# Optimization experiments

Hardware: AMD Instinct MI355X
Metric: run time of the kernel (lower is better)

## Reference

```python
import jax, jax.numpy as jnp
import numpy as np

N_HEADS = 8
D_HEAD = 64


def setup_inputs() -> dict:
    key = jax.random.key(0)
    ks = jax.random.split(key, 7)
    B, Sq, Dm = 16, 4096, 512
    Skv, Dc = 77, 768
    inner = N_HEADS * D_HEAD  # 512
    s = lambda d: 1.0 / np.sqrt(d)
    return {
        "x": jax.random.normal(ks[0], (B, Sq, Dm), jnp.float32),
        "context": jax.random.normal(ks[1], (B, Skv, Dc), jnp.float32),
        "Wq": jax.random.normal(ks[2], (Dm, inner), jnp.float32) * s(Dm),
        "Wk": jax.random.normal(ks[3], (Dc, inner), jnp.float32) * s(Dc),
        "Wv": jax.random.normal(ks[4], (Dc, inner), jnp.float32) * s(Dc),
        "Wout": jax.random.normal(ks[5], (inner, inner), jnp.float32) * s(inner),
        "bout": jnp.zeros((inner,), jnp.float32),
    }


def reference(x, context, Wq, Wk, Wv, Wout, bout):
    B, Sq, _ = x.shape
    Skv = context.shape[1]
    scale = D_HEAD ** (-0.5)
    # projections (no bias)
    q = (x @ Wq).reshape(B, Sq, N_HEADS, D_HEAD)
    k = (context @ Wk).reshape(B, Skv, N_HEADS, D_HEAD)
    v = (context @ Wv).reshape(B, Skv, N_HEADS, D_HEAD)
    # scores: [B, H, Sq, Skv]
    score = jnp.einsum("bqhd,bkhd->bhqk", q, k) * scale
    weights = jax.nn.softmax(score, axis=-1)
    attn = jnp.einsum("bhqk,bkhd->bqhd", weights, v)
    h = attn.reshape(B, Sq, N_HEADS * D_HEAD)
    return h @ Wout + bout
```

## Files before the change

kernel.cpp:

```cpp
#include <hip/hip_runtime.h>


typedef unsigned short u16;
typedef unsigned int u32;
typedef _Float16 f16;
typedef __attribute__((ext_vector_type(8))) _Float16 half8;
typedef __attribute__((ext_vector_type(4))) _Float16 half4;
typedef __attribute__((ext_vector_type(4))) float f32x4;

__device__ __forceinline__ f32x4 mfma16h(half8 a, half8 b, f32x4 c) {
    return __builtin_amdgcn_mfma_f32_16x16x32_f16(a, b, c, 0, 0, 0);
}
__device__ __forceinline__ void gl_lds16(const f16* g, f16* l) {
    __builtin_amdgcn_global_load_lds(
        (const __attribute__((address_space(1))) void*)g,
        (__attribute__((address_space(3))) void*)l, 16, 0, 0);
}

__global__ __launch_bounds__(256) void prep(
    const float* __restrict__ Wq, const float* __restrict__ Wk,
    const float* __restrict__ Wv, const float* __restrict__ Wo,
    f16* __restrict__ WqT, f16* __restrict__ WkT,
    f16* __restrict__ WvT, f16* __restrict__ WoT,
    f16* __restrict__ vT, f16* __restrict__ kbuf)
{
    int idx = blockIdx.x * 256 + threadIdx.x;
    if (idx < 1310720) {
        const float* W; f16* T; int K; int base;
        if (idx < 262144)        { W = Wq; T = WqT; K = 512; base = 0; }
        else if (idx < 655360)   { W = Wk; T = WkT; K = 768; base = 262144; }
        else if (idx < 1048576)  { W = Wv; T = WvT; K = 768; base = 655360; }
        else                     { W = Wo; T = WoT; K = 512; base = 1048576; }
        int j = idx - base;
        int n = j / K, k = j - n * K;
        T[j] = (f16)W[(size_t)k * 512 + n];
        return;
    }
    int i = idx - 1310720;
    const int nv = 16 * 512 * 19;
    if (i < nv) {
        int g = i / 19, s = i - g * 19;
        vT[(size_t)g * 96 + 77 + s] = (f16)0.f;
    } else {
        int j = i - nv;
        if (j < 8 * 512) kbuf[(size_t)1232 * 512 + j] = (f16)0.f;
    }
}

__global__ __launch_bounds__(256, 2) void kvx(
    const float* __restrict__ ctx, const f16* __restrict__ Bkv,
    f16* __restrict__ kbuf, f16* __restrict__ vT,
    const float* __restrict__ x, const f16* __restrict__ WqT,
    f16* __restrict__ qh)
{
    __shared__ f16 smem[24576];

    const int bid = blockIdx.x;
    const int t = threadIdx.x;
    const int lane = t & 63;
    const int w = t >> 6;
    const int ar = lane & 15;
    const int kc = (lane >> 4) << 3;

    if (bid < 320) {
        f16* lA = smem;
        f16* lB = smem + 2560;

        const int wr = w >> 1, wc = w & 1;
        const int m0 = (bid % 20) * 64, n0 = (bid / 20) * 64;

        const int srow = t >> 2;
        const int sc8  = (t & 3) << 3;

        f32x4 acc[2][2] = {};

        for (int k0 = 0; k0 < 768; k0 += 32) {
            float4 v0 = make_float4(0.f, 0.f, 0.f, 0.f);
            float4 v1 = make_float4(0.f, 0.f, 0.f, 0.f);
            int gr = m0 + srow;
            if (gr < 1232) {
                v0 = *(const float4*)(ctx + (size_t)gr * 768 + k0 + sc8);
                v1 = *(const float4*)(ctx + (size_t)gr * 768 + k0 + sc8 + 4);
            }
            half8 ha = {(f16)v0.x, (f16)v0.y, (f16)v0.z, (f16)v0.w,
                        (f16)v1.x, (f16)v1.y, (f16)v1.z, (f16)v1.w};
            *(half8*)(lA + srow * 40 + sc8) = ha;
            *(half8*)(lB + srow * 40 + sc8) =
                *(const half8*)(Bkv + (size_t)(n0 + srow) * 768 + k0 + sc8);
            __syncthreads();

            half8 fa[2], fb[2];
            #pragma unroll
            for (int m = 0; m < 2; ++m)
                fa[m] = *(const half8*)(lA + (wr * 32 + m * 16 + ar) * 40 + kc);
            #pragma unroll
            for (int n = 0; n < 2; ++n)
                fb[n] = *(const half8*)(lB + (wc * 32 + n * 16 + ar) * 40 + kc);
            #pragma unroll
            for (int m = 0; m < 2; ++m)
                #pragma unroll
                for (int n = 0; n < 2; ++n)
                    acc[m][n] = mfma16h(fa[m], fb[n], acc[m][n]);
            __syncthreads();
        }

        #pragma unroll
        for (int n = 0; n < 2; ++n) {
            int col = n0 + wc * 32 + n * 16 + ar;
            #pragma unroll
            for (int m = 0; m < 2; ++m) {
                #pragma unroll
                for (int r = 0; r < 4; ++r) {
                    int row = m0 + wr * 32 + m * 16 + ((lane >> 4) << 2) + r;
                    if (row < 1232) {
                        f16 v = (f16)acc[m][n][r];
                        if (col < 512) {
                            kbuf[(size_t)row * 512 + col] = v;
                        } else {
                            int bb = row / 77;
                            int si = row - bb * 77;
                            vT[((size_t)bb * 512 + (col - 512)) * 96 + si] = v;
                        }
                    }
                }
            }
        }
        return;
    }

    f16* sA0 = smem;
    f16* sB0 = smem + 8192;

    const int wr = w >> 1, wc = w & 1;

    const int f = bid - 320;
    const int logical = (f & 7) * 128 + (f >> 3);
    const int m0 = (logical >> 1) * 128;
    const int n0 = (logical & 1) * 256;

    const int arow = t >> 3;
    const int acol = (t & 7) << 2;
    const int brow = lane >> 2;
    const int bcol = (lane & 3) << 3;

    f32x4 acc[4][8] = {};
    f32x4 rA[4];

    auto LOAD_A = [&](int kt) {
        #pragma unroll
        for (int j = 0; j < 4; ++j)
            rA[j] = *(const f32x4*)(x + (size_t)(m0 + arow + j * 32) * 512
                                      + (kt << 5) + acol);
    };
    auto WRITE_A = [&](int buf) {
        #pragma unroll
        for (int j = 0; j < 4; ++j) {
            half4 h = {(f16)rA[j].x, (f16)rA[j].y, (f16)rA[j].z, (f16)rA[j].w};
            *(half4*)(sA0 + buf * 4096 + (arow + j * 32) * 32 + acol) = h;
        }
    };
    auto STAGE_B = [&](int buf, int kt) {
        #pragma unroll
        for (int j = 0; j < 4; ++j) {
            const int ci = w * 4 + j;
            gl_lds16(WqT + (size_t)(n0 + ci * 16 + brow) * 512 + (kt << 5) + bcol,
                     sB0 + buf * 8192 + ci * 512);
        }
    };

    LOAD_A(0);
    STAGE_B(0, 0);
    WRITE_A(0);
    __syncthreads();

    int cur = 0;
    for (int kt = 0; kt < 16; ++kt) {
        if (kt + 1 < 16) {
            LOAD_A(kt + 1);
            STAGE_B(cur ^ 1, kt + 1);
        }

        half8 fa[4], fb[8];
        #pragma unroll
        for (int m = 0; m < 4; ++m)
            fa[m] = *(const half8*)(sA0 + cur * 4096 + (wr * 64 + m * 16 + ar) * 32 + kc);
        #pragma unroll
        for (int n = 0; n < 8; ++n)
            fb[n] = *(const half8*)(sB0 + cur * 8192 + (wc * 128 + n * 16 + ar) * 32 + kc);

        __builtin_amdgcn_s_setprio(1);
        #pragma unroll
        for (int m = 0; m < 4; ++m)
            #pragma unroll
            for (int n = 0; n < 8; ++n)
                acc[m][n] = mfma16h(fa[m], fb[n], acc[m][n]);
        __builtin_amdgcn_s_setprio(0);

        if (kt + 1 < 16) WRITE_A(cur ^ 1);
        __syncthreads();
        cur ^= 1;
    }

    #pragma unroll
    for (int n = 0; n < 8; ++n) {
        int col = n0 + wc * 128 + n * 16 + ar;
        #pragma unroll
        for (int m = 0; m < 4; ++m) {
            #pragma unroll
            for (int r = 0; r < 4; ++r) {
                int row = m0 + wr * 64 + m * 16 + ((lane >> 4) << 2) + r;
                qh[(size_t)row * 512 + col] = (f16)acc[m][n][r];
            }
        }
    }
}

__global__ __launch_bounds__(256, 2) void gemm_h16(
    const f16* __restrict__ A, const f16* __restrict__ B,
    const float* __restrict__ bias, float* __restrict__ C,
    int M, int N, int K)
{
    __shared__ f16 sA[2][128 * 32];
    __shared__ f16 sB[2][256 * 32];

    const int t = threadIdx.x;
    const int lane = t & 63;
    const int w = t >> 6;
    const int wr = w >> 1, wc = w & 1;

    const int f = blockIdx.x + gridDim.x * blockIdx.y;
    const int cpx = (gridDim.x * gridDim.y) >> 3;
    const int logical = (f & 7) * cpx + (f >> 3);
    const int m0 = (logical / gridDim.x) * 128;
    const int n0 = (logical % gridDim.x) * 256;

    const int ar = lane & 15;
    const int kc = (lane >> 4) << 3;
    const int srow = lane >> 2;
    const int scol = (lane & 3) << 3;

    f32x4 acc[4][8] = {};

    auto STAGE = [&](int buf, int kt) {
        #pragma unroll
        for (int j = 0; j < 2; ++j) {
            const int ci = w * 2 + j;
            gl_lds16(A + (size_t)(m0 + ci * 16 + srow) * K + (kt << 5) + scol,
                     &sA[buf][ci * 512]);
        }
        #pragma unroll
        for (int j = 0; j < 4; ++j) {
            const int ci = w * 4 + j;
            gl_lds16(B + (size_t)(n0 + ci * 16 + srow) * K + (kt << 5) + scol,
                     &sB[buf][ci * 512]);
        }
    };

    const int nk = K >> 5;
    STAGE(0, 0);
    __syncthreads();

    int cur = 0;
    for (int kt = 0; kt < nk; ++kt) {
        if (kt + 1 < nk) STAGE(cur ^ 1, kt + 1);

        half8 fa[4], fb[8];
        #pragma unroll
        for (int m = 0; m < 4; ++m)
            fa[m] = *(const half8*)(&sA[cur][(wr * 64 + m * 16 + ar) * 32 + kc]);
        #pragma unroll
        for (int n = 0; n < 8; ++n)
            fb[n] = *(const half8*)(&sB[cur][(wc * 128 + n * 16 + ar) * 32 + kc]);

        __builtin_amdgcn_s_setprio(1);
        #pragma unroll
        for (int m = 0; m < 4; ++m)
            #pragma unroll
            for (int n = 0; n < 8; ++n)
                acc[m][n] = mfma16h(fa[m], fb[n], acc[m][n]);
        __builtin_amdgcn_s_setprio(0);
        __syncthreads();
        cur ^= 1;
    }

    #pragma unroll
    for (int n = 0; n < 8; ++n) {
        int col = n0 + wc * 128 + n * 16 + ar;
        float bv = bias[col];
        #pragma unroll
        for (int m = 0; m < 4; ++m) {
            #pragma unroll
            for (int r = 0; r < 4; ++r) {
                int row = m0 + wr * 64 + m * 16 + ((lane >> 4) << 2) + r;
                C[(size_t)row * N + col] = acc[m][n][r] + bv;
            }
        }
    }
}

__global__ __launch_bounds__(256) void attn_h16(
    const f16* __restrict__ q, const f16* __restrict__ k,
    const f16* __restrict__ vT, f16* __restrict__ outA)
{
    constexpr int PST = 104;
    __shared__ f16 sP[4 * 32 * PST];

    const int t = threadIdx.x;
    const int lane = t & 63;
    const int w = t >> 6;
    const int ar = lane & 15;
    const int kg = lane >> 4;
    const int kc = kg << 3;
    const int b = blockIdx.z, head = blockIdx.y;
    const size_t qrow0 = (size_t)b * 4096 + blockIdx.x * 128 + w * 32;

    f32x4 accs[2][5] = {};
    #pragma unroll
    for (int ks = 0; ks < 2; ++ks) {
        const int d = head * 64 + ks * 32 + kc;
        half8 ah[2];
        #pragma unroll
        for (int m = 0; m < 2; ++m)
            ah[m] = *(const half8*)(q + (qrow0 + m * 16 + ar) * 512 + d);
        #pragma unroll
        for (int n = 0; n < 5; ++n) {
            half8 bh = *(const half8*)(k + ((size_t)(b * 77 + n * 16 + ar)) * 512 + d);
            #pragma unroll
            for (int m = 0; m < 2; ++m)
                accs[m][n] = mfma16h(ah[m], bh, accs[m][n]);
        }
    }

    #pragma unroll
    for (int m = 0; m < 2; ++m) {
        #pragma unroll
        for (int r = 0; r < 4; ++r) {
            float mx = -1e30f;
            #pragma unroll
            for (int n = 0; n < 5; ++n) {
                float v = accs[m][n][r] * 0.125f;
                if (n == 4 && ar >= 13) v = -1e30f;
                accs[m][n][r] = v;
                mx = fmaxf(mx, v);
            }
            mx = fmaxf(mx, __shfl_xor(mx, 1));
            mx = fmaxf(mx, __shfl_xor(mx, 2));
            mx = fmaxf(mx, __shfl_xor(mx, 4));
            mx = fmaxf(mx, __shfl_xor(mx, 8));
            float sum = 0.f;
            #pragma unroll
            for (int n = 0; n < 5; ++n) {
                float e = __expf(accs[m][n][r] - mx);
                accs[m][n][r] = e;
                sum += e;
            }
            sum += __shfl_xor(sum, 1);
            sum += __shfl_xor(sum, 2);
            sum += __shfl_xor(sum, 4);
            sum += __shfl_xor(sum, 8);
            float inv = 1.f / sum;
            #pragma unroll
            for (int n = 0; n < 5; ++n) accs[m][n][r] *= inv;
        }
    }

    f16* myP = sP + w * 32 * PST;
    for (int i = lane; i < 32 * 12; i += 64) {
        int row = i / 12, c = 80 + (i % 12) * 2;
        *(u32*)(myP + row * PST + c) = 0;
    }
    #pragma unroll
    for (int m = 0; m < 2; ++m)
        #pragma unroll
        for (int n = 0; n < 5; ++n)
            #pragma unroll
            for (int r = 0; r < 4; ++r)
                myP[(m * 16 + kg * 4 + r) * PST + n * 16 + ar] = (f16)accs[m][n][r];

    f32x4 accp[2][4] = {};
    #pragma unroll
    for (int ks = 0; ks < 3; ++ks) {
        half8 pa[2];
        #pragma unroll
        for (int m = 0; m < 2; ++m)
            pa[m] = *(const half8*)(myP + (m * 16 + ar) * PST + ks * 32 + kc);
        #pragma unroll
        for (int n = 0; n < 4; ++n) {
            half8 bh = *(const half8*)(vT + ((size_t)b * 512 + head * 64 + n * 16 + ar) * 96 + ks * 32 + kc);
            #pragma unroll
            for (int m = 0; m < 2; ++m)
                accp[m][n] = mfma16h(pa[m], bh, accp[m][n]);
        }
    }

    #pragma unroll
    for (int m = 0; m < 2; ++m)
        #pragma unroll
        for (int n = 0; n < 4; ++n)
            #pragma unroll
            for (int r = 0; r < 4; ++r)
                outA[(qrow0 + m * 16 + kg * 4 + r) * 512 + head * 64 + n * 16 + ar]
                    = (f16)accp[m][n][r];
}

extern "C" void kernel_launch(void* const* d_in, const int* in_sizes, int n_in,
                              void* d_out, int out_size, void* d_ws, size_t ws_size,
                              hipStream_t stream)
{
    const float* x    = (const float*)d_in[0];
    const float* ctx  = (const float*)d_in[1];
    const float* Wq   = (const float*)d_in[2];
    const float* Wk   = (const float*)d_in[3];
    const float* Wv   = (const float*)d_in[4];
    const float* Wout = (const float*)d_in[5];
    const float* bout = (const float*)d_in[6];

    char* ws = (char*)d_ws;
    size_t off = 0;
    auto alloc = [&](size_t bytes) -> void* {
        void* p = ws + off;
        off += (bytes + 255) & ~(size_t)255;
        return p;
    };
    f16* WqT = (f16*)alloc(512 * 512 * 2);
    f16* WkT = (f16*)alloc(768 * 512 * 2);
    f16* WvT = (f16*)alloc(768 * 512 * 2);
    f16* WoT = (f16*)alloc(512 * 512 * 2);
    f16* kbuf = (f16*)alloc((size_t)1240 * 512 * 2);
    f16* vT   = (f16*)alloc((size_t)16 * 512 * 96 * 2);
    f16* qh   = (f16*)alloc((size_t)65536 * 512 * 2);
    f16* attnA = (f16*)alloc((size_t)65536 * 512 * 2);
    (void)ws_size; (void)in_sizes; (void)n_in; (void)out_size;

    prep<<<dim3(5744), dim3(256), 0, stream>>>(
        Wq, Wk, Wv, Wout, WqT, WkT, WvT, WoT, vT, kbuf);

    kvx<<<dim3(1344), dim3(256), 0, stream>>>(
        ctx, WkT, kbuf, vT, x, WqT, qh);

    attn_h16<<<dim3(32, 8, 16), dim3(256), 0, stream>>>(qh, kbuf, vT, attnA);

    gemm_h16<<<dim3(2, 512), dim3(256), 0, stream>>>(
        attnA, WoT, bout, (float*)d_out, 65536, 512, 512);
}
```

Baseline: 210.2 us.

## Double-buffer and register-prefetch the K/V projection GEMM with 64-wide K tiles

The context K/V projection branch of the kvx kernel now loads the next 64-wide K slice into registers while MFMAs run on the current LDS buffer. Results are written to a second LDS buffer, so each step needs one barrier instead of two. This hides global load latency and halves the loop trip count. In exchange it uses more LDS (18432 f16 in the A/B tiles, within the existing 24576) and more registers for the prefetch, which may pressure occupancy at launch bounds of 2 blocks.

```diff
diff --git a/kernel.cpp b/kernel.cpp
--- a/kernel.cpp
+++ b/kernel.cpp
@@ -64,44 +64,72 @@
 
     if (bid < 320) {
         f16* lA = smem;
-        f16* lB = smem + 2560;
+        f16* lB = smem + 9216;
 
         const int wr = w >> 1, wc = w & 1;
         const int m0 = (bid % 20) * 64, n0 = (bid / 20) * 64;
 
         const int srow = t >> 2;
-        const int sc8  = (t & 3) << 3;
+        const int sc   = (t & 3) << 4;
 
         f32x4 acc[2][2] = {};
-
-        for (int k0 = 0; k0 < 768; k0 += 32) {
-            float4 v0 = make_float4(0.f, 0.f, 0.f, 0.f);
-            float4 v1 = make_float4(0.f, 0.f, 0.f, 0.f);
-            int gr = m0 + srow;
+        f32x4 rA[4];
+        half8 rB[2];
+
+        auto LOAD_KV = [&](int kt) {
+            const int gr = m0 + srow;
             if (gr < 1232) {
-                v0 = *(const float4*)(ctx + (size_t)gr * 768 + k0 + sc8);
-                v1 = *(const float4*)(ctx + (size_t)gr * 768 + k0 + sc8 + 4);
-            }
-            half8 ha = {(f16)v0.x, (f16)v0.y, (f16)v0.z, (f16)v0.w,
-                        (f16)v1.x, (f16)v1.y, (f16)v1.z, (f16)v1.w};
-            *(half8*)(lA + srow * 40 + sc8) = ha;
-            *(half8*)(lB + srow * 40 + sc8) =
-                *(const half8*)(Bkv + (size_t)(n0 + srow) * 768 + k0 + sc8);
+                const float* pa = ctx + (size_t)gr * 768 + (kt << 6) + sc;
+                #pragma unroll
+                for (int j = 0; j < 4; ++j) rA[j] = *(const f32x4*)(pa + j * 4);
+            } else {
+                #pragma unroll
+                for (int j = 0; j < 4; ++j) rA[j] = (f32x4){0.f, 0.f, 0.f, 0.f};
+            }
+            const f16* pb = Bkv + (size_t)(n0 + srow) * 768 + (kt << 6) + sc;
+            rB[0] = *(const half8*)(pb);
+            rB[1] = *(const half8*)(pb + 8);
+        };
+        auto WRITE_KV = [&](int buf) {
+            half8 h0 = { (f16)rA[0].x, (f16)rA[0].y, (f16)rA[0].z, (f16)rA[0].w,
+                         (f16)rA[1].x, (f16)rA[1].y, (f16)rA[1].z, (f16)rA[1].w };
+            half8 h1 = { (f16)rA[2].x, (f16)rA[2].y, (f16)rA[2].z, (f16)rA[2].w,
+                         (f16)rA[3].x, (f16)rA[3].y, (f16)rA[3].z, (f16)rA[3].w };
+            *(half8*)(lA + buf * 4608 + srow * 72 + sc)     = h0;
+            *(half8*)(lA + buf * 4608 + srow * 72 + sc + 8) = h1;
+            *(half8*)(lB + buf * 4608 + srow * 72 + sc)     = rB[0];
+            *(half8*)(lB + buf * 4608 + srow * 72 + sc + 8) = rB[1];
+        };
+
+        LOAD_KV(0);
+        WRITE_KV(0);
+        __syncthreads();
+
+        int cur = 0;
+        for (int kt = 0; kt < 12; ++kt) {
+            if (kt + 1 < 12) LOAD_KV(kt + 1);
+
+            #pragma unroll
+            for (int ks = 0; ks < 2; ++ks) {
+                half8 fa[2], fb[2];
+                #pragma unroll
+                for (int m = 0; m < 2; ++m)
+                    fa[m] = *(const half8*)(lA + cur * 4608
+                                + (wr * 32 + m * 16 + ar) * 72 + ks * 32 + kc);
+                #pragma unroll
+                for (int n = 0; n < 2; ++n)
+                    fb[n] = *(const half8*)(lB + cur * 4608
+                                + (wc * 32 + n * 16 + ar) * 72 + ks * 32 + kc);
+                #pragma unroll
+                for (int m = 0; m < 2; ++m)
+                    #pragma unroll
+                    for (int n = 0; n < 2; ++n)
+                        acc[m][n] = mfma16h(fa[m], fb[n], acc[m][n]);
+            }
+
+            if (kt + 1 < 12) WRITE_KV(cur ^ 1);
             __syncthreads();
-
-            half8 fa[2], fb[2];
-            #pragma unroll
-            for (int m = 0; m < 2; ++m)
-                fa[m] = *(const half8*)(lA + (wr * 32 + m * 16 + ar) * 40 + kc);
-            #pragma unroll
-            for (int n = 0; n < 2; ++n)
-                fb[n] = *(const half8*)(lB + (wc * 32 + n * 16 + ar) * 40 + kc);
-            #pragma unroll
-            for (int m = 0; m < 2; ++m)
-                #pragma unroll
-                for (int n = 0; n < 2; ++n)
-                    acc[m][n] = mfma16h(fa[m], fb[n], acc[m][n]);
-            __syncthreads();
+            cur ^= 1;
         }
 
         #pragma unroll
```

After: 203.9 us. 3.0% less time.
